# Kernel tuning notes

Measured on AMD Instinct MI355X. Metric: run time of the kernel, lower is better.

Reference implementation:

```python
import jax, jax.numpy as jnp
import numpy as np

B, N_VIS = 2, 512
T, HP, WP = 8, 16, 16
L = T * HP * WP              # 2048 tokens
D, HEAD_DIM = 384, 48
N_HEADS = D // HEAD_DIM      # 8
N_LAYERS, F_DIM = 8, 1536
EPS = 1e-6
THETA = 10000.0


def _rms(x, w):
    return x * jax.lax.rsqrt(jnp.mean(x * x, axis=-1, keepdims=True) + EPS) * w


def _rope_cos_sin(t, h, w):
    # VideoRotaryEmbeddingSplit466: split head_dim//2 freqs 4:6:6 over (t,h,w)
    half = HEAD_DIM // 2
    inv = 1.0 / (THETA ** (jnp.arange(half, dtype=jnp.float32) / half))
    dt = half * 4 // 16
    dh = half * 6 // 16
    l = jnp.arange(t * h * w)
    tp = l // (h * w)
    rem = l % (h * w)
    hp = rem // w
    wp = rem % w
    f = jnp.concatenate([tp[:, None] * inv[:dt],
                         hp[:, None] * inv[dt:dt + dh],
                         wp[:, None] * inv[dt + dh:]], axis=1)   # (L, half)
    emb = jnp.concatenate([f, f], axis=-1)                        # (L, HEAD_DIM)
    return jnp.cos(emb), jnp.sin(emb)


def _rot_half(x):
    x1, x2 = jnp.split(x, 2, axis=-1)
    return jnp.concatenate([-x2, x1], axis=-1)


def _forward(visible_embeddings, ids_restore, mask, t_frames, h_patches, w_patches,
             mask_token, ln_in_w, ln1_w, ln2_w, Wq, bq, Wk, bk, Wv, bv, Wo, bo,
             W1, b1, W2, b2):
    b, n_vis, d = visible_embeddings.shape
    l_full = ids_restore.shape[1]
    ppf = h_patches * w_patches
    n_mask = l_full - n_vis
    # append learnable mask tokens and un-shuffle with ids_restore
    x_cat = jnp.concatenate(
        [visible_embeddings, jnp.broadcast_to(mask_token, (b, n_mask, d))], axis=1)
    x_full = jnp.take_along_axis(x_cat, ids_restore[:, :, None].astype(jnp.int32), axis=1)
    # 3D RoPE over full grid
    cos, sin = _rope_cos_sin(t_frames, h_patches, w_patches)      # (L, HEAD_DIM)
    # frame-level mask, True = forbid. Faithful to torch broadcasting:
    # forbid[i, j] = frame_ids[j] < frame_ids[i]
    fid = jnp.arange(l_full) // ppf
    forbid = fid[None, :] < fid[:, None]                          # (L, L)
    bias = jnp.where(forbid, jnp.finfo(jnp.float32).min, 0.0)
    # pre-norm transformer stack (RMSNorm, exact GELU MLP)
    x = _rms(x_full, ln_in_w)
    scale = 1.0 / jnp.sqrt(jnp.float32(HEAD_DIM))
    cs = cos[None, :, None, :]
    sn = sin[None, :, None, :]
    for i in range(N_LAYERS):
        hdn = _rms(x, ln1_w[i])
        q = (hdn @ Wq[i] + bq[i]).reshape(b, l_full, N_HEADS, HEAD_DIM)
        k = (hdn @ Wk[i] + bk[i]).reshape(b, l_full, N_HEADS, HEAD_DIM)
        v = (hdn @ Wv[i] + bv[i]).reshape(b, l_full, N_HEADS, HEAD_DIM)
        q = q * cs + _rot_half(q) * sn
        k = k * cs + _rot_half(k) * sn
        s = jnp.einsum('bqhd,bkhd->bhqk', q, k) * scale + bias
        a = jax.nn.softmax(s, axis=-1)
        o = jnp.einsum('bhqk,bkhd->bqhd', a, v).reshape(b, l_full, d)
        x = x + o @ Wo[i] + bo[i]
        h2 = _rms(x, ln2_w[i])
        x = x + jax.nn.gelu(h2 @ W1[i] + b1[i], approximate=False) @ W2[i] + b2[i]
    decoded_full = x  # feature_head = Identity (feature_proj_dim is None)
    # split visible / masked: every row has exactly n_vis ones -> static shapes
    order = jnp.argsort(-mask, axis=1, stable=True)               # visible first, in order
    decoded_visible = jnp.take_along_axis(decoded_full, order[:, :n_vis, None], axis=1)
    decoded_masked = jnp.take_along_axis(decoded_full, order[:, n_vis:, None], axis=1)
    return decoded_full, decoded_visible, decoded_masked


def setup_inputs():
    key = jax.random.key(0)
    ks = jax.random.split(key, 12)
    vis = jax.random.normal(ks[0], (B, N_VIS, D), jnp.float32)
    noise = jax.random.uniform(ks[1], (B, L))
    ids_shuffle = jnp.argsort(noise, axis=1)
    ids_restore = jnp.argsort(ids_shuffle, axis=1).astype(jnp.int32)
    mask = jnp.zeros((B, L), jnp.int32).at[
        jnp.arange(B)[:, None], ids_shuffle[:, :N_VIS]].set(1)    # 1 = visible

    def p(k, shape):
        return jax.random.normal(k, shape, jnp.float32) * 0.02

    return {
        'visible_embeddings': vis, 'ids_restore': ids_restore, 'mask': mask,
        't_frames': T, 'h_patches': HP, 'w_patches': WP,
        'mask_token': p(ks[2], (D,)),
        'ln_in_w': jnp.ones((D,), jnp.float32),
        'ln1_w': jnp.ones((N_LAYERS, D), jnp.float32),
        'ln2_w': jnp.ones((N_LAYERS, D), jnp.float32),
        'Wq': p(ks[3], (N_LAYERS, D, D)), 'bq': jnp.zeros((N_LAYERS, D)),
        'Wk': p(ks[4], (N_LAYERS, D, D)), 'bk': jnp.zeros((N_LAYERS, D)),
        'Wv': p(ks[5], (N_LAYERS, D, D)), 'bv': jnp.zeros((N_LAYERS, D)),
        'Wo': p(ks[6], (N_LAYERS, D, D)), 'bo': jnp.zeros((N_LAYERS, D)),
        'W1': p(ks[7], (N_LAYERS, D, F_DIM)), 'b1': jnp.zeros((N_LAYERS, F_DIM)),
        'W2': p(ks[8], (N_LAYERS, F_DIM, D)), 'b2': jnp.zeros((N_LAYERS, D)),
    }


def reference(visible_embeddings, ids_restore, mask, t_frames, h_patches, w_patches,
              mask_token, ln_in_w, ln1_w, ln2_w, Wq, bq, Wk, bk, Wv, bv, Wo, bo,
              W1, b1, W2, b2):
    return _forward(visible_embeddings, ids_restore, mask, t_frames, h_patches,
                    w_patches, mask_token, ln_in_w, ln1_w, ln2_w, Wq, bq, Wk, bk,
                    Wv, bv, Wo, bo, W1, b1, W2, b2)
```

## Files before the change

kernel.cpp:

```cpp
#include <hip/hip_runtime.h>

typedef __attribute__((ext_vector_type(8))) __bf16 bf16x8;
typedef __attribute__((ext_vector_type(8))) unsigned short ushort8;
typedef __attribute__((ext_vector_type(4))) float floatx4;

#define NB 2
#define SEQ 2048
#define DIM 384
#define NH 8
#define HD 48
#define HDP 64
#define FF 1536
#define NLAYER 8
#define ATT_SCALE 0.14433756729740643f

__device__ __forceinline__ unsigned short f2bf(float f) {
  unsigned u = __builtin_bit_cast(unsigned, f);
  u += 0x7fffu + ((u >> 16) & 1u);
  return (unsigned short)(u >> 16);
}
__device__ __forceinline__ float bf2f(unsigned short h) {
  unsigned u = ((unsigned)h) << 16;
  return __builtin_bit_cast(float, u);
}
__device__ __forceinline__ bf16x8 ldb8(const unsigned short* p) {
  return __builtin_bit_cast(bf16x8, *(const ushort8*)p);
}
__device__ __forceinline__ void gl2lds16(const unsigned short* g, unsigned short* l) {
  __builtin_amdgcn_global_load_lds((const __attribute__((address_space(1))) unsigned int*)g,
                                   (__attribute__((address_space(3))) unsigned int*)l, 16, 0, 0);
}
#define MFMA(a, b, c) __builtin_amdgcn_mfma_f32_16x16x32_bf16(a, b, c, 0, 0, 0)

__global__ __launch_bounds__(256) void wtrans_kernel(const float* __restrict__ W,
                                                     unsigned short* __restrict__ Wt,
                                                     int K, int N,
                                                     size_t sstride, size_t dstride) {
  __shared__ unsigned short tile[32][33];
  const float* Wl = W + (size_t)blockIdx.z * sstride;
  unsigned short* Wtl = Wt + (size_t)blockIdx.z * dstride;
  int n0 = blockIdx.x * 32, k0 = blockIdx.y * 32;
  int tx = threadIdx.x, ty = threadIdx.y;
  for (int i = ty; i < 32; i += 8)
    tile[i][tx] = f2bf(Wl[(size_t)(k0 + i) * N + n0 + tx]);
  __syncthreads();
  for (int i = ty; i < 32; i += 8)
    Wtl[(size_t)(n0 + i) * K + k0 + tx] = tile[tx][i];
}

__global__ void biascat_kernel(const float* __restrict__ bq, const float* __restrict__ bk,
                               const float* __restrict__ bv, float* __restrict__ out) {
  int idx = blockIdx.x * 256 + threadIdx.x;
  if (idx >= NLAYER * 1152) return;
  int z = idx / 1152, j = idx % 1152;
  float v = (j < 384) ? bq[z * 384 + j] : (j < 768) ? bk[z * 384 + j - 384] : bv[z * 384 + j - 768];
  out[idx] = v;
}

__global__ void ropetab_kernel(float* __restrict__ cosT, float* __restrict__ sinT) {
  int idx = blockIdx.x * 256 + threadIdx.x;
  if (idx >= SEQ * HD) return;
  int l = idx / HD, d = idx % HD;
  int j = d % 24;
  float inv = powf(10000.0f, -(float)j / 24.0f);
  float pos;
  if (j < 6) pos = (float)(l >> 8);
  else if (j < 15) pos = (float)((l >> 4) & 15);
  else pos = (float)(l & 15);
  float f = pos * inv;
  cosT[idx] = cosf(f);
  sinT[idx] = sinf(f);
}

__global__ __launch_bounds__(256) void gatherrms_kernel(const float* __restrict__ vis,
                                                        const int* __restrict__ ids,
                                                        const float* __restrict__ mask_token,
                                                        const float* __restrict__ w,
                                                        float* __restrict__ x) {
  int wv = threadIdx.x >> 6, lane = threadIdx.x & 63;
  int row = blockIdx.x * 4 + wv;
  int b = row >> 11;
  int src = ids[row];
  const float* p = (src < 512) ? (vis + ((size_t)b * 512 + src) * DIM) : mask_token;
  float v[6];
  float ss = 0.f;
#pragma unroll
  for (int j = 0; j < 6; j++) { v[j] = p[lane + 64 * j]; ss += v[j] * v[j]; }
#pragma unroll
  for (int m = 32; m; m >>= 1) ss += __shfl_xor(ss, m);
  float s = rsqrtf(ss * (1.0f / DIM) + 1e-6f);
#pragma unroll
  for (int j = 0; j < 6; j++)
    x[(size_t)row * DIM + lane + 64 * j] = v[j] * s * w[lane + 64 * j];
}

__global__ __launch_bounds__(256) void rmsadd_kernel(float* __restrict__ x,
                                                     const float* __restrict__ p0,
                                                     const float* __restrict__ p1,
                                                     const float* __restrict__ w,
                                                     unsigned short* __restrict__ out,
                                                     int doadd) {
  int wv = threadIdx.x >> 6, lane = threadIdx.x & 63;
  int row = blockIdx.x * 4 + wv;
  size_t base = (size_t)row * DIM;
  float v[6];
  float ss = 0.f;
  if (doadd) {
#pragma unroll
    for (int j = 0; j < 6; j++) {
      int o = lane + 64 * j;
      v[j] = x[base + o] + p0[base + o] + p1[base + o];
      x[base + o] = v[j];
      ss += v[j] * v[j];
    }
  } else {
#pragma unroll
    for (int j = 0; j < 6; j++) { v[j] = x[base + lane + 64 * j]; ss += v[j] * v[j]; }
  }
#pragma unroll
  for (int m = 32; m; m >>= 1) ss += __shfl_xor(ss, m);
  float s = rsqrtf(ss * (1.0f / DIM) + 1e-6f);
#pragma unroll
  for (int j = 0; j < 6; j++)
    out[base + lane + 64 * j] = f2bf(v[j] * s * w[lane + 64 * j]);
}

__global__ __launch_bounds__(256) void gemm64_kernel(const unsigned short* __restrict__ A,
                                                     const unsigned short* __restrict__ Wt,
                                                     const float* __restrict__ bias,
                                                     int M, int N, int K, int mode,
                                                     unsigned short* __restrict__ outb,
                                                     unsigned short* __restrict__ outb2,
                                                     unsigned short* __restrict__ outv,
                                                     float* __restrict__ outf0,
                                                     float* __restrict__ outf1) {
  __shared__ __align__(16) unsigned short As[64 * 32];
  __shared__ __align__(16) unsigned short Bs[64 * 32];
  int tid = threadIdx.x;
  int wv = tid >> 6, lane = tid & 63;
  int wm = wv >> 1, wn = wv & 1;
  int row0 = blockIdx.x * 64, col0 = blockIdx.y * 64;
  int q = lane >> 4, c = lane & 15;
  int kchunk = K / gridDim.z;
  int kb0 = blockIdx.z * kchunk;
  floatx4 acc[2][2] = {};
  int sr = tid >> 2, sk = (tid & 3) * 8;
  const unsigned short* Ag = A + (size_t)(row0 + sr) * K + kb0 + sk;
  const unsigned short* Bg = Wt + (size_t)(col0 + sr) * K + kb0 + sk;
  unsigned short* Asl = As + tid * 8;
  unsigned short* Bsl = Bs + tid * 8;
  for (int k0 = 0; k0 < kchunk; k0 += 32) {
    gl2lds16(Ag + k0, Asl);
    gl2lds16(Bg + k0, Bsl);
    __syncthreads();
    bf16x8 a0 = ldb8(&As[(wm * 32 + c) * 32 + q * 8]);
    bf16x8 a1 = ldb8(&As[(wm * 32 + 16 + c) * 32 + q * 8]);
    bf16x8 b0 = ldb8(&Bs[(wn * 32 + c) * 32 + q * 8]);
    bf16x8 b1 = ldb8(&Bs[(wn * 32 + 16 + c) * 32 + q * 8]);
    acc[0][0] = MFMA(a0, b0, acc[0][0]);
    acc[0][1] = MFMA(a0, b1, acc[0][1]);
    acc[1][0] = MFMA(a1, b0, acc[1][0]);
    acc[1][1] = MFMA(a1, b1, acc[1][1]);
    __syncthreads();
  }
  float* outf = blockIdx.z ? outf1 : outf0;
  int addb = (blockIdx.z == 0);
#pragma unroll
  for (int tm = 0; tm < 2; tm++)
#pragma unroll
    for (int tn = 0; tn < 2; tn++)
#pragma unroll
      for (int r = 0; r < 4; r++) {
        int rg = row0 + wm * 32 + tm * 16 + q * 4 + r;
        int cg = col0 + wn * 32 + tn * 16 + c;
        float v = acc[tm][tn][r] + (addb ? bias[cg] : 0.f);
        if (mode == 3) {
          float g = v * 0.5f * (1.0f + erff(v * 0.70710678f));
          outb[(size_t)rg * N + cg] = f2bf(g);
        } else if (mode == 4) {
          if (cg < 384) {
            outb[(size_t)rg * 384 + cg] = f2bf(v);
          } else if (cg < 768) {
            outb2[(size_t)rg * 384 + cg - 384] = f2bf(v);
          } else {
            int j = cg - 768;
            int h = j / HD, hd = j % HD;
            int b = rg >> 11, l = rg & 2047;
            outv[(((size_t)b * NH + h) * HDP + hd) * SEQ + l] = f2bf(v);
          }
        } else {
          outf[(size_t)rg * N + cg] = v;
        }
      }
}

__global__ __launch_bounds__(384) void rope_kernel(const unsigned short* __restrict__ qpre,
                                                   const unsigned short* __restrict__ kpre,
                                                   const float* __restrict__ cosT,
                                                   const float* __restrict__ sinT,
                                                   unsigned short* __restrict__ qdst,
                                                   unsigned short* __restrict__ kdst) {
  int row = blockIdx.x;
  int b = row >> 11, l = row & 2047;
  int t = threadIdx.x;
  const unsigned short* src = (t >= 192) ? kpre : qpre;
  unsigned short* dst = (t >= 192) ? kdst : qdst;
  float sc = (t >= 192) ? 1.0f : ATT_SCALE;
  int pp = t % 192;
  int h = pp / 24, d = pp % 24;
  float x1 = bf2f(src[(size_t)row * DIM + h * HD + d]);
  float x2 = bf2f(src[(size_t)row * DIM + h * HD + d + 24]);
  float cs = cosT[l * HD + d], sn = sinT[l * HD + d];
  size_t base = (((size_t)b * NH + h) * SEQ + l) * HDP;
  dst[base + d] = f2bf((x1 * cs - x2 * sn) * sc);
  dst[base + d + 24] = f2bf((x2 * cs + x1 * sn) * sc);
}

__global__ __launch_bounds__(256) void fattn_kernel(const unsigned short* __restrict__ qb,
                                                    const unsigned short* __restrict__ kb,
                                                    const unsigned short* __restrict__ vt,
                                                    unsigned short* __restrict__ obuf) {
  __shared__ __align__(16) unsigned short Ks[64][72];
  __shared__ __align__(16) unsigned short Vs[48][72];
  __shared__ __align__(16) unsigned short Pt[4][16][72];
  int tid = threadIdx.x;
  int wv = tid >> 6, lane = tid & 63;
  int q = lane >> 4, c = lane & 15;
  int i = blockIdx.x;
  int bh = 2 * (i & 7) + ((i >> 3) & 1);
  int q0 = (i >> 4) * 64;
  int kstart = q0 & ~255;
  const unsigned short* qbase = qb + (size_t)bh * SEQ * HDP;
  const unsigned short* kbase = kb + (size_t)bh * SEQ * HDP;
  const unsigned short* vbase = vt + (size_t)bh * HDP * SEQ;
  int myrow = q0 + wv * 16;
  bf16x8 a0 = ldb8(qbase + (size_t)(myrow + c) * HDP + q * 8);
  bf16x8 a1 = ldb8(qbase + (size_t)(myrow + c) * HDP + 32 + q * 8);
  floatx4 O[3] = {};
  float mr[4] = {-3e38f, -3e38f, -3e38f, -3e38f};
  float lr[4] = {0.f, 0.f, 0.f, 0.f};
  int srow = tid >> 2, schunk = (tid & 3) * 16;
  for (int k0 = kstart; k0 < SEQ; k0 += 64) {
    const unsigned short* kg = kbase + (size_t)(k0 + srow) * HDP + schunk;
    *(ushort8*)(&Ks[srow][schunk]) = *(const ushort8*)kg;
    *(ushort8*)(&Ks[srow][schunk + 8]) = *(const ushort8*)(kg + 8);
    if (srow < 48) {
      const unsigned short* vg = vbase + (size_t)srow * SEQ + k0 + schunk;
      *(ushort8*)(&Vs[srow][schunk]) = *(const ushort8*)vg;
      *(ushort8*)(&Vs[srow][schunk + 8]) = *(const ushort8*)(vg + 8);
    }
    __syncthreads();
    floatx4 S[4];
#pragma unroll
    for (int t = 0; t < 4; t++) {
      bf16x8 b0 = ldb8(&Ks[t * 16 + c][q * 8]);
      bf16x8 b1 = ldb8(&Ks[t * 16 + c][32 + q * 8]);
      floatx4 z = {};
      z = MFMA(a0, b0, z);
      S[t] = MFMA(a1, b1, z);
    }
    float alpha[4];
#pragma unroll
    for (int r = 0; r < 4; r++) {
      float m0 = fmaxf(fmaxf(S[0][r], S[1][r]), fmaxf(S[2][r], S[3][r]));
#pragma unroll
      for (int msk = 1; msk < 16; msk <<= 1) m0 = fmaxf(m0, __shfl_xor(m0, msk, 16));
      float nm = fmaxf(mr[r], m0);
      alpha[r] = __expf(mr[r] - nm);
      mr[r] = nm;
      lr[r] *= alpha[r];
    }
#pragma unroll
    for (int t = 0; t < 4; t++)
#pragma unroll
      for (int r = 0; r < 4; r++) {
        float pv = __expf(S[t][r] - mr[r]);
        lr[r] += pv;
        Pt[wv][q * 4 + r][t * 16 + c] = f2bf(pv);
      }
#pragma unroll
    for (int f = 0; f < 3; f++)
#pragma unroll
      for (int r = 0; r < 4; r++) O[f][r] *= alpha[r];
    bf16x8 pa0 = ldb8(&Pt[wv][c][q * 8]);
    bf16x8 pa1 = ldb8(&Pt[wv][c][32 + q * 8]);
#pragma unroll
    for (int f = 0; f < 3; f++) {
      bf16x8 v0 = ldb8(&Vs[f * 16 + c][q * 8]);
      bf16x8 v1 = ldb8(&Vs[f * 16 + c][32 + q * 8]);
      O[f] = MFMA(pa0, v0, O[f]);
      O[f] = MFMA(pa1, v1, O[f]);
    }
    __syncthreads();
  }
#pragma unroll
  for (int r = 0; r < 4; r++) {
#pragma unroll
    for (int msk = 1; msk < 16; msk <<= 1) lr[r] += __shfl_xor(lr[r], msk, 16);
    lr[r] = 1.0f / lr[r];
  }
  int b = bh >> 3, h = bh & 7;
#pragma unroll
  for (int f = 0; f < 3; f++)
#pragma unroll
    for (int r = 0; r < 4; r++)
      obuf[((size_t)b * SEQ + myrow + q * 4 + r) * DIM + h * HD + f * 16 + c] =
          f2bf(O[f][r] * lr[r]);
}

__global__ __launch_bounds__(256) void rank_kernel(const int* __restrict__ mask,
                                                   int* __restrict__ dest) {
  __shared__ int wsum[4];
  int b = blockIdx.x, t = threadIdx.x;
  int lane = t & 63, wv = t >> 6;
  const int* mb = mask + b * SEQ;
  int base = t * 8;
  int v[8];
  int s = 0;
#pragma unroll
  for (int j = 0; j < 8; j++) { v[j] = mb[base + j]; s += v[j]; }
  int incl = s;
  for (int off = 1; off < 64; off <<= 1) {
    int n = __shfl_up(incl, off);
    if (lane >= off) incl += n;
  }
  if (lane == 63) wsum[wv] = incl;
  __syncthreads();
  int P = incl - s;
  for (int w = 0; w < wv; w++) P += wsum[w];
  int run = 0;
#pragma unroll
  for (int j = 0; j < 8; j++) {
    int ones = P + run;
    int l = base + j;
    dest[b * SEQ + l] = v[j] ? ones : 512 + (l - ones);
    run += v[j];
  }
}

__global__ __launch_bounds__(256) void output_kernel(const float* __restrict__ x,
                                                     const float* __restrict__ p0,
                                                     const float* __restrict__ p1,
                                                     const int* __restrict__ dest,
                                                     float* __restrict__ out) {
  int idx = blockIdx.x * 256 + threadIdx.x;
  int row = idx / 96, c = idx % 96;
  size_t base_i = (size_t)row * DIM;
  float4 v = ((const float4*)(x + base_i))[c];
  float4 a = ((const float4*)(p0 + base_i))[c];
  float4 bb = ((const float4*)(p1 + base_i))[c];
  v.x += a.x + bb.x; v.y += a.y + bb.y; v.z += a.z + bb.z; v.w += a.w + bb.w;
  ((float4*)(out + base_i))[c] = v;
  int b = row >> 11;
  int d = dest[row];
  size_t base = (size_t)NB * SEQ * DIM;
  size_t o;
  if (d < 512) o = base + ((size_t)b * 512 + d) * DIM;
  else o = base + (size_t)NB * 512 * DIM + ((size_t)b * 1536 + (d - 512)) * DIM;
  ((float4*)(out + o))[c] = v;
}

extern "C" void kernel_launch(void* const* d_in, const int* in_sizes, int n_in,
                              void* d_out, int out_size, void* d_ws, size_t ws_size,
                              hipStream_t stream) {
  const float* vis = (const float*)d_in[0];
  const int* ids = (const int*)d_in[1];
  const int* mask = (const int*)d_in[2];
  const float* mask_token = (const float*)d_in[6];
  const float* ln_in_w = (const float*)d_in[7];
  const float* ln1_w = (const float*)d_in[8];
  const float* ln2_w = (const float*)d_in[9];
  const float* Wq = (const float*)d_in[10];
  const float* bq = (const float*)d_in[11];
  const float* Wk = (const float*)d_in[12];
  const float* bk = (const float*)d_in[13];
  const float* Wv = (const float*)d_in[14];
  const float* bv = (const float*)d_in[15];
  const float* Wo = (const float*)d_in[16];
  const float* bo = (const float*)d_in[17];
  const float* W1 = (const float*)d_in[18];
  const float* b1 = (const float*)d_in[19];
  const float* W2 = (const float*)d_in[20];
  const float* b2 = (const float*)d_in[21];

  char* p = (char*)d_ws;
  size_t off = 0;
  auto alloc = [&](size_t n) -> void* {
    off = (off + 255) & ~(size_t)255;
    void* r = p + off;
    off += n;
    return r;
  };
  unsigned short* wqkvT = (unsigned short*)alloc((size_t)NLAYER * 1152 * DIM * 2);
  unsigned short* woT = (unsigned short*)alloc((size_t)NLAYER * DIM * DIM * 2);
  unsigned short* w1T = (unsigned short*)alloc((size_t)NLAYER * DIM * FF * 2);
  unsigned short* w2T = (unsigned short*)alloc((size_t)NLAYER * DIM * FF * 2);
  float* bqkv = (float*)alloc((size_t)NLAYER * 1152 * 4);
  float* cosT = (float*)alloc((size_t)SEQ * HD * 4);
  float* sinT = (float*)alloc((size_t)SEQ * HD * 4);
  float* x = (float*)alloc((size_t)NB * SEQ * DIM * 4);
  unsigned short* hdn = (unsigned short*)alloc((size_t)NB * SEQ * DIM * 2);
  unsigned short* qpre = (unsigned short*)alloc((size_t)NB * SEQ * DIM * 2);
  unsigned short* kpre = (unsigned short*)alloc((size_t)NB * SEQ * DIM * 2);
  unsigned short* qb = (unsigned short*)alloc((size_t)NB * NH * SEQ * HDP * 2);
  unsigned short* kb = (unsigned short*)alloc((size_t)NB * NH * SEQ * HDP * 2);
  unsigned short* vtb = (unsigned short*)alloc((size_t)NB * NH * SEQ * HDP * 2);
  unsigned short* obuf = (unsigned short*)alloc((size_t)NB * SEQ * DIM * 2);
  unsigned short* a1 = (unsigned short*)alloc((size_t)NB * SEQ * FF * 2);
  float* pA0 = (float*)alloc((size_t)NB * SEQ * DIM * 4);
  float* pA1 = (float*)alloc((size_t)NB * SEQ * DIM * 4);
  float* pB0 = (float*)alloc((size_t)NB * SEQ * DIM * 4);
  float* pB1 = (float*)alloc((size_t)NB * SEQ * DIM * 4);
  int* dest = (int*)alloc((size_t)NB * SEQ * 4);

  hipMemsetAsync(qb, 0, (size_t)NB * NH * SEQ * HDP * 2, stream);
  hipMemsetAsync(kb, 0, (size_t)NB * NH * SEQ * HDP * 2, stream);

  dim3 tb(32, 8);
  wtrans_kernel<<<dim3(12, 12, 8), tb, 0, stream>>>(Wq, wqkvT, 384, 384, 147456, 442368);
  wtrans_kernel<<<dim3(12, 12, 8), tb, 0, stream>>>(Wk, wqkvT + 147456, 384, 384, 147456, 442368);
  wtrans_kernel<<<dim3(12, 12, 8), tb, 0, stream>>>(Wv, wqkvT + 294912, 384, 384, 147456, 442368);
  wtrans_kernel<<<dim3(12, 12, 8), tb, 0, stream>>>(Wo, woT, 384, 384, 147456, 147456);
  wtrans_kernel<<<dim3(48, 12, 8), tb, 0, stream>>>(W1, w1T, 384, 1536, 589824, 589824);
  wtrans_kernel<<<dim3(12, 48, 8), tb, 0, stream>>>(W2, w2T, 1536, 384, 589824, 589824);
  biascat_kernel<<<(NLAYER * 1152 + 255) / 256, 256, 0, stream>>>(bq, bk, bv, bqkv);
  ropetab_kernel<<<(SEQ * HD + 255) / 256, 256, 0, stream>>>(cosT, sinT);
  gatherrms_kernel<<<NB * SEQ / 4, 256, 0, stream>>>(vis, ids, mask_token, ln_in_w, x);

  for (int i = 0; i < NLAYER; i++) {
    size_t wo = (size_t)i * DIM * DIM;
    size_t wf = (size_t)i * DIM * FF;
    rmsadd_kernel<<<NB * SEQ / 4, 256, 0, stream>>>(x, pB0, pB1, ln1_w + i * DIM, hdn, i > 0);
    gemm64_kernel<<<dim3(64, 18, 1), 256, 0, stream>>>(hdn, wqkvT + (size_t)i * 442368,
                                                       bqkv + i * 1152, NB * SEQ, 1152, DIM, 4,
                                                       qpre, kpre, vtb, nullptr, nullptr);
    rope_kernel<<<NB * SEQ, 384, 0, stream>>>(qpre, kpre, cosT, sinT, qb, kb);
    fattn_kernel<<<512, 256, 0, stream>>>(qb, kb, vtb, obuf);
    gemm64_kernel<<<dim3(64, 6, 2), 256, 0, stream>>>(obuf, woT + wo, bo + i * DIM, NB * SEQ, DIM,
                                                      DIM, 5, nullptr, nullptr, nullptr, pA0, pA1);
    rmsadd_kernel<<<NB * SEQ / 4, 256, 0, stream>>>(x, pA0, pA1, ln2_w + i * DIM, hdn, 1);
    gemm64_kernel<<<dim3(64, 24, 1), 256, 0, stream>>>(hdn, w1T + wf, b1 + i * FF, NB * SEQ, FF,
                                                       DIM, 3, a1, nullptr, nullptr, nullptr,
                                                       nullptr);
    gemm64_kernel<<<dim3(64, 6, 2), 256, 0, stream>>>(a1, w2T + wf, b2 + i * DIM, NB * SEQ, DIM,
                                                      FF, 5, nullptr, nullptr, nullptr, pB0, pB1);
  }
  rank_kernel<<<NB, 256, 0, stream>>>(mask, dest);
  output_kernel<<<NB * SEQ * 96 / 256, 256, 0, stream>>>(x, pB0, pB1, dest, (float*)d_out);
}
```

Measured before the change: 1.149 ms.

## Split attention KV range in two with merge kernel and double-buffered K/V tiles

The attention kernel now splits each query block's key range into two halves, launched as separate blocks, so twice as many workgroups run. Each half writes unnormalized fp32 partial outputs plus its row max and row sum, and a new merge kernel combines them into the bf16 output. K/V tiles are now prefetched into registers and double-buffered in shared memory, which lets one barrier per iteration be dropped. The cost is an extra kernel launch and several megabytes of fp32 partial traffic per layer.

New measurement: 1.053 ms. 1.09x faster.

```diff
diff --git a/kernel.cpp b/kernel.cpp
--- a/kernel.cpp
+++ b/kernel.cpp
@@ -219,17 +219,25 @@
 __global__ __launch_bounds__(256) void fattn_kernel(const unsigned short* __restrict__ qb,
                                                     const unsigned short* __restrict__ kb,
                                                     const unsigned short* __restrict__ vt,
-                                                    unsigned short* __restrict__ obuf) {
-  __shared__ __align__(16) unsigned short Ks[64][72];
-  __shared__ __align__(16) unsigned short Vs[48][72];
-  __shared__ __align__(16) unsigned short Pt[4][16][72];
+                                                    float* __restrict__ pO,
+                                                    float* __restrict__ pM,
+                                                    float* __restrict__ pL) {
+  __shared__ __align__(16) unsigned short Ks[2][64][72];
+  __shared__ __align__(16) unsigned short Vs[2][48][72];
+  __shared__ __align__(16) unsigned short Pt[4][16][64];
   int tid = threadIdx.x;
   int wv = tid >> 6, lane = tid & 63;
   int q = lane >> 4, c = lane & 15;
   int i = blockIdx.x;
   int bh = 2 * (i & 7) + ((i >> 3) & 1);
-  int q0 = (i >> 4) * 64;
+  int rest = i >> 4;
+  int z = rest & 1;
+  int q0 = (rest >> 1) * 64;
   int kstart = q0 & ~255;
+  int n = (SEQ - kstart) >> 6;
+  int n2 = (n + 1) >> 1;
+  int it0 = z * n2;
+  int it1 = z ? n : n2;
   const unsigned short* qbase = qb + (size_t)bh * SEQ * HDP;
   const unsigned short* kbase = kb + (size_t)bh * SEQ * HDP;
   const unsigned short* vbase = vt + (size_t)bh * HDP * SEQ;
@@ -239,25 +247,45 @@
   floatx4 O[3] = {};
   float mr[4] = {-3e38f, -3e38f, -3e38f, -3e38f};
   float lr[4] = {0.f, 0.f, 0.f, 0.f};
-  int srow = tid >> 2, schunk = (tid & 3) * 16;
-  for (int k0 = kstart; k0 < SEQ; k0 += 64) {
-    const unsigned short* kg = kbase + (size_t)(k0 + srow) * HDP + schunk;
-    *(ushort8*)(&Ks[srow][schunk]) = *(const ushort8*)kg;
-    *(ushort8*)(&Ks[srow][schunk + 8]) = *(const ushort8*)(kg + 8);
+  int srow = tid >> 2, sch = (tid & 3) * 16;
+  ushort8 kA, kB, vA, vB;
+  const unsigned short* kg0 = kbase + (size_t)srow * HDP + sch;
+  const unsigned short* vg0 = vbase + (size_t)srow * SEQ + sch;
+  {
+    int k0 = kstart + it0 * 64;
+    kA = *(const ushort8*)(kg0 + (size_t)k0 * HDP);
+    kB = *(const ushort8*)(kg0 + (size_t)k0 * HDP + 8);
     if (srow < 48) {
-      const unsigned short* vg = vbase + (size_t)srow * SEQ + k0 + schunk;
-      *(ushort8*)(&Vs[srow][schunk]) = *(const ushort8*)vg;
-      *(ushort8*)(&Vs[srow][schunk + 8]) = *(const ushort8*)(vg + 8);
+      vA = *(const ushort8*)(vg0 + k0);
+      vB = *(const ushort8*)(vg0 + k0 + 8);
+    }
+  }
+  for (int it = it0; it < it1; ++it) {
+    int buf = it & 1;
+    *(ushort8*)(&Ks[buf][srow][sch]) = kA;
+    *(ushort8*)(&Ks[buf][srow][sch + 8]) = kB;
+    if (srow < 48) {
+      *(ushort8*)(&Vs[buf][srow][sch]) = vA;
+      *(ushort8*)(&Vs[buf][srow][sch + 8]) = vB;
+    }
+    if (it + 1 < it1) {
+      int k0 = kstart + (it + 1) * 64;
+      kA = *(const ushort8*)(kg0 + (size_t)k0 * HDP);
+      kB = *(const ushort8*)(kg0 + (size_t)k0 * HDP + 8);
+      if (srow < 48) {
+        vA = *(const ushort8*)(vg0 + k0);
+        vB = *(const ushort8*)(vg0 + k0 + 8);
+      }
     }
     __syncthreads();
     floatx4 S[4];
 #pragma unroll
     for (int t = 0; t < 4; t++) {
-      bf16x8 b0 = ldb8(&Ks[t * 16 + c][q * 8]);
-      bf16x8 b1 = ldb8(&Ks[t * 16 + c][32 + q * 8]);
-      floatx4 z = {};
-      z = MFMA(a0, b0, z);
-      S[t] = MFMA(a1, b1, z);
+      bf16x8 b0 = ldb8(&Ks[buf][t * 16 + c][q * 8]);
+      bf16x8 b1 = ldb8(&Ks[buf][t * 16 + c][32 + q * 8]);
+      floatx4 zz = {};
+      zz = MFMA(a0, b0, zz);
+      S[t] = MFMA(a1, b1, zz);
     }
     float alpha[4];
 #pragma unroll
@@ -286,26 +314,44 @@
     bf16x8 pa1 = ldb8(&Pt[wv][c][32 + q * 8]);
 #pragma unroll
     for (int f = 0; f < 3; f++) {
-      bf16x8 v0 = ldb8(&Vs[f * 16 + c][q * 8]);
-      bf16x8 v1 = ldb8(&Vs[f * 16 + c][32 + q * 8]);
+      bf16x8 v0 = ldb8(&Vs[buf][f * 16 + c][q * 8]);
+      bf16x8 v1 = ldb8(&Vs[buf][f * 16 + c][32 + q * 8]);
       O[f] = MFMA(pa0, v0, O[f]);
       O[f] = MFMA(pa1, v1, O[f]);
     }
-    __syncthreads();
-  }
+  }
+#pragma unroll
+  for (int r = 0; r < 4; r++)
+#pragma unroll
+    for (int msk = 1; msk < 16; msk <<= 1) lr[r] += __shfl_xor(lr[r], msk, 16);
+  size_t pbase = (size_t)z * (NB * NH * SEQ) + (size_t)bh * SEQ + myrow;
 #pragma unroll
   for (int r = 0; r < 4; r++) {
-#pragma unroll
-    for (int msk = 1; msk < 16; msk <<= 1) lr[r] += __shfl_xor(lr[r], msk, 16);
-    lr[r] = 1.0f / lr[r];
-  }
-  int b = bh >> 3, h = bh & 7;
-#pragma unroll
-  for (int f = 0; f < 3; f++)
-#pragma unroll
-    for (int r = 0; r < 4; r++)
-      obuf[((size_t)b * SEQ + myrow + q * 4 + r) * DIM + h * HD + f * 16 + c] =
-          f2bf(O[f][r] * lr[r]);
+    int row = q * 4 + r;
+    if (c == 0) {
+      pM[pbase + row] = mr[r];
+      pL[pbase + row] = lr[r];
+    }
+#pragma unroll
+    for (int f = 0; f < 3; f++) pO[(pbase + row) * 48 + f * 16 + c] = O[f][r];
+  }
+}
+
+__global__ __launch_bounds__(256) void amerge_kernel(const float* __restrict__ pO,
+                                                     const float* __restrict__ pM,
+                                                     const float* __restrict__ pL,
+                                                     unsigned short* __restrict__ obuf) {
+  int idx = blockIdx.x * 256 + threadIdx.x;
+  int rowg = idx / 48, d = idx - rowg * 48;
+  const int NR = NB * NH * SEQ;
+  float m0 = pM[rowg], m1 = pM[NR + rowg];
+  float l0 = pL[rowg], l1 = pL[NR + rowg];
+  float M = fmaxf(m0, m1);
+  float e0 = __expf(m0 - M), e1 = __expf(m1 - M);
+  float inv = 1.0f / (l0 * e0 + l1 * e1);
+  float v = (pO[(size_t)rowg * 48 + d] * e0 + pO[(size_t)(NR + rowg) * 48 + d] * e1) * inv;
+  int bh = rowg >> 11, l = rowg & 2047;
+  obuf[(((size_t)(bh >> 3)) * SEQ + l) * DIM + (bh & 7) * HD + d] = f2bf(v);
 }
 
 __global__ __launch_bounds__(256) void rank_kernel(const int* __restrict__ mask,
@@ -411,6 +457,9 @@
   float* pA1 = (float*)alloc((size_t)NB * SEQ * DIM * 4);
   float* pB0 = (float*)alloc((size_t)NB * SEQ * DIM * 4);
   float* pB1 = (float*)alloc((size_t)NB * SEQ * DIM * 4);
+  float* pO = (float*)alloc((size_t)2 * NB * NH * SEQ * 48 * 4);
+  float* pM = (float*)alloc((size_t)2 * NB * NH * SEQ * 4);
+  float* pL = (float*)alloc((size_t)2 * NB * NH * SEQ * 4);
   int* dest = (int*)alloc((size_t)NB * SEQ * 4);
 
   hipMemsetAsync(qb, 0, (size_t)NB * NH * SEQ * HDP * 2, stream);
@@ -435,7 +484,8 @@
                                                        bqkv + i * 1152, NB * SEQ, 1152, DIM, 4,
                                                        qpre, kpre, vtb, nullptr, nullptr);
     rope_kernel<<<NB * SEQ, 384, 0, stream>>>(qpre, kpre, cosT, sinT, qb, kb);
-    fattn_kernel<<<512, 256, 0, stream>>>(qb, kb, vtb, obuf);
+    fattn_kernel<<<1024, 256, 0, stream>>>(qb, kb, vtb, pO, pM, pL);
+    amerge_kernel<<<NB * NH * SEQ * 48 / 256, 256, 0, stream>>>(pO, pM, pL, obuf);
     gemm64_kernel<<<dim3(64, 6, 2), 256, 0, stream>>>(obuf, woT + wo, bo + i * DIM, NB * SEQ, DIM,
                                                       DIM, 5, nullptr, nullptr, nullptr, pA0, pA1);
     rmsadd_kernel<<<NB * SEQ / 4, 256, 0, stream>>>(x, pA0, pA1, ln2_w + i * DIM, hdn, 1);
```
